# Optimization experiments

Measured on AMD Instinct MI355X. Metric: run time of the kernel, lower is better.

## Reference

```python
import jax, jax.numpy as jnp
import numpy as np

N_NODES = 100000
N_EDGES = 640000
F = 128          # in_features
MID = 192        # (2*F + OUT)//2
OUT = 128


def setup_inputs() -> dict:
    key = jax.random.key(0)
    k_h, k_dr, k_s, k_d, k_w1, k_w2 = jax.random.split(key, 6)
    h = jax.random.normal(k_h, (N_NODES, F), dtype=jnp.float32)
    dR = jax.random.uniform(k_dr, (N_EDGES,), dtype=jnp.float32)
    src_idx = jax.random.randint(k_s, (N_EDGES,), 0, N_NODES)
    dst_idx = jax.random.randint(k_d, (N_EDGES,), 0, N_NODES)
    W1 = jax.random.normal(k_w1, (2 * F + 1, MID), dtype=jnp.float32) * (1.0 / np.sqrt(2 * F + 1))
    b1 = jnp.zeros((MID,), dtype=jnp.float32)
    W2 = jax.random.normal(k_w2, (MID, OUT), dtype=jnp.float32) * (1.0 / np.sqrt(MID))
    b2 = jnp.zeros((OUT,), dtype=jnp.float32)
    return {"h": h, "dR": dR, "src_idx": src_idx, "dst_idx": dst_idx,
            "W1": W1, "b1": b1, "W2": W2, "b2": b2}


def reference(h, dR, src_idx, dst_idx, W1, b1, W2, b2):
    # first=True branch: cat([dst_hidden, src_hidden, dR[:, None]]) -> [E, 2F+1]
    inp = jnp.concatenate([h[dst_idx], h[src_idx], dR[:, None]], axis=1)
    hid = jax.nn.relu(inp @ W1 + b1)          # [E, MID]
    out = jnp.tanh(hid @ W2 + b2)             # [E, OUT]
    return out
```

## Files before the change

### kernel.cpp

```cpp
#include <hip/hip_runtime.h>


#define F_IN   128
#define MID    192
#define OUT_N  128
#define K1     256
#define M_TILE 64
#define H_STRIDE 200

typedef __attribute__((ext_vector_type(8))) short bf16x8;
typedef __attribute__((ext_vector_type(8))) unsigned short u16x8;
typedef __attribute__((ext_vector_type(4))) float f32x4;

__device__ __forceinline__ unsigned short f2bf(float f) {
    unsigned u = __builtin_bit_cast(unsigned, f);
    u = (u + 0x7FFFu + ((u >> 16) & 1u)) >> 16;
    return (unsigned short)u;
}

__global__ void pack_weights(const float* __restrict__ W1,
                             const float* __restrict__ W2,
                             unsigned short* __restrict__ p1,
                             unsigned short* __restrict__ p2,
                             float* __restrict__ wdr) {
    int i = blockIdx.x * 256 + threadIdx.x;
    if (i < K1 * MID) {
        int kin = i & 31;
        int rest = i >> 5;
        int n = rest % MID;
        int kt = rest / MID;
        p1[i] = f2bf(W1[(kt * 32 + kin) * MID + n]);
    }
    int j = i - K1 * MID;
    if (j >= 0 && j < MID * OUT_N) {
        int kin = j & 31;
        int rest = j >> 5;
        int n = rest & 127;
        int kt = rest >> 7;
        p2[j] = f2bf(W2[(kt * 32 + kin) * OUT_N + n]);
    }
    if (i < MID) wdr[i] = W1[256 * MID + i];
}

__global__ void hconv(const float* __restrict__ h,
                      unsigned short* __restrict__ hb, int n8) {
    int i = blockIdx.x * 256 + threadIdx.x;
    if (i >= n8) return;
    const float4* hp = (const float4*)h;
    float4 v0 = hp[2 * i];
    float4 v1 = hp[2 * i + 1];
    u16x8 o;
    o[0] = f2bf(v0.x); o[1] = f2bf(v0.y); o[2] = f2bf(v0.z); o[3] = f2bf(v0.w);
    o[4] = f2bf(v1.x); o[5] = f2bf(v1.y); o[6] = f2bf(v1.z); o[7] = f2bf(v1.w);
    *((u16x8*)hb + i) = o;
}

__global__ __launch_bounds__(256, 5)
void edge_mlp_kernel(const unsigned short* __restrict__ hb,
                     const float* __restrict__ dR,
                     const int*   __restrict__ src_idx,
                     const int*   __restrict__ dst_idx,
                     const float* __restrict__ b1,
                     const float* __restrict__ b2,
                     const unsigned short* __restrict__ p1,
                     const unsigned short* __restrict__ p2,
                     const float* __restrict__ wdr,
                     float* __restrict__ out) {
    __shared__ __align__(16) unsigned short sA[M_TILE * 256];

    const int tid  = threadIdx.x;
    const int lane = tid & 63;
    const int w    = tid >> 6;
    const int e0   = blockIdx.x * M_TILE;

    const float dr_own = dR[e0 + lane];

    {
        const int g = lane >> 4;
        const int c = lane & 15;
        const int part = g & 1;
        const int* __restrict__ ip = part ? src_idx : dst_idx;
        const int eb = w * 16 + (g >> 1);
        int rows[8];
#pragma unroll
        for (int i = 0; i < 8; ++i) rows[i] = ip[e0 + eb + 2 * i];
#pragma unroll
        for (int i = 0; i < 8; ++i) {
            const int el = eb + 2 * i;
            const unsigned short* gp =
                hb + ((size_t)rows[i] << 7) + ((c ^ (el & 7)) << 3);
            unsigned short* lp = &sA[(w * 16 + 2 * i) * 256];
            __builtin_amdgcn_global_load_lds(
                (const __attribute__((address_space(1))) void*)gp,
                (__attribute__((address_space(3))) void*)lp,
                16, 0, 0);
        }
    }
    __syncthreads();

    const int l15 = lane & 15;
    const int q   = lane >> 4;

    f32x4 acc1[4][3] = {};
    for (int kt = 0; kt < 8; ++kt) {
        bf16x8 a[4];
#pragma unroll
        for (int m = 0; m < 4; ++m) {
            const int r = m * 16 + l15;
            a[m] = *(const bf16x8*)(&sA[r * 256 + (((kt * 4 + q) ^ (r & 7)) << 3)]);
        }
#pragma unroll
        for (int ni = 0; ni < 3; ++ni) {
            const int nb = (w + ni * 4) * 16 + l15;
            bf16x8 bf = *(const bf16x8*)(&p1[((kt * MID + nb) << 5) + (q << 3)]);
#pragma unroll
            for (int m = 0; m < 4; ++m)
                acc1[m][ni] = __builtin_amdgcn_mfma_f32_16x16x32_bf16(a[m], bf, acc1[m][ni], 0, 0, 0);
        }
    }
    __syncthreads();

    float drv[16];
#pragma unroll
    for (int m = 0; m < 4; ++m)
#pragma unroll
        for (int r = 0; r < 4; ++r)
            drv[m * 4 + r] = __shfl(dr_own, m * 16 + q * 4 + r);

    unsigned short* sH = sA;
#pragma unroll
    for (int ni = 0; ni < 3; ++ni) {
        const int n = (w + ni * 4) * 16 + l15;
        const float bb = b1[n];
        const float wd = wdr[n];
#pragma unroll
        for (int m = 0; m < 4; ++m) {
#pragma unroll
            for (int r = 0; r < 4; ++r) {
                const int e = m * 16 + q * 4 + r;
                float v = acc1[m][ni][r] + bb + drv[m * 4 + r] * wd;
                v = fmaxf(v, 0.0f);
                sH[e * H_STRIDE + n] = f2bf(v);
            }
        }
    }
    __syncthreads();

    f32x4 acc2[4][2] = {};
    for (int kt = 0; kt < 6; ++kt) {
        bf16x8 a[4];
#pragma unroll
        for (int m = 0; m < 4; ++m)
            a[m] = *(const bf16x8*)(&sH[(m * 16 + l15) * H_STRIDE + kt * 32 + q * 8]);
#pragma unroll
        for (int ni = 0; ni < 2; ++ni) {
            const int nb = (w + ni * 4) * 16 + l15;
            bf16x8 bf = *(const bf16x8*)(&p2[((kt * OUT_N + nb) << 5) + (q << 3)]);
#pragma unroll
            for (int m = 0; m < 4; ++m)
                acc2[m][ni] = __builtin_amdgcn_mfma_f32_16x16x32_bf16(a[m], bf, acc2[m][ni], 0, 0, 0);
        }
    }

#pragma unroll
    for (int ni = 0; ni < 2; ++ni) {
        const int n = (w + ni * 4) * 16 + l15;
        const float bb = b2[n];
#pragma unroll
        for (int m = 0; m < 4; ++m) {
#pragma unroll
            for (int r = 0; r < 4; ++r) {
                const int e = e0 + m * 16 + q * 4 + r;
                float x = acc2[m][ni][r] + bb;
                x = fminf(fmaxf(x, -10.0f), 10.0f);
                float t = __expf(2.0f * x);
                float y = (t - 1.0f) * __builtin_amdgcn_rcpf(t + 1.0f);
                __builtin_nontemporal_store(y, &out[(size_t)e * OUT_N + n]);
            }
        }
    }
}

extern "C" void kernel_launch(void* const* d_in, const int* in_sizes, int n_in,
                              void* d_out, int out_size, void* d_ws, size_t ws_size,
                              hipStream_t stream) {
    const float* h   = (const float*)d_in[0];
    const float* dR  = (const float*)d_in[1];
    const int* src   = (const int*)d_in[2];
    const int* dst   = (const int*)d_in[3];
    const float* W1  = (const float*)d_in[4];
    const float* b1  = (const float*)d_in[5];
    const float* W2  = (const float*)d_in[6];
    const float* b2  = (const float*)d_in[7];
    float* out       = (float*)d_out;

    const int hn = in_sizes[0];
    const int E  = in_sizes[1];

    unsigned short* hbuf = (unsigned short*)d_ws;
    unsigned short* p1   = hbuf + hn;
    unsigned short* p2   = p1 + K1 * MID;
    float* wdr           = (float*)(p2 + MID * OUT_N);

    hconv<<<(hn / 8 + 255) / 256, 256, 0, stream>>>(h, hbuf, hn / 8);
    pack_weights<<<(K1 * MID + MID * OUT_N + 255) / 256, 256, 0, stream>>>(W1, W2, p1, p2, wdr);
    edge_mlp_kernel<<<E / M_TILE, 256, 0, stream>>>(hbuf, dR, src, dst, b1, b2, p1, p2, wdr, out);
}
```

Baseline: 503.9 us.

## Make edge MLP persistent with double-buffered gather and register-resident weights

Converts the edge MLP kernel into a persistent grid of 512 blocks that loop over tiles, prefetching the next tile's gathered node rows into a second LDS buffer while computing the current one. W1/W2 fragments and biases are loaded once into registers per block instead of per tile. This aims to hide gather latency and remove repeated weight loads, at the cost of high register pressure (occupancy lowered to 2 blocks per CU), doubled LDS, and dropping the nontemporal output stores.

```diff
diff --git a/kernel.cpp b/kernel.cpp
--- a/kernel.cpp
+++ b/kernel.cpp
@@ -7,6 +7,7 @@
 #define K1     256
 #define M_TILE 64
 #define H_STRIDE 200
+#define NBLK   512
 
 typedef __attribute__((ext_vector_type(8))) short bf16x8;
 typedef __attribute__((ext_vector_type(8))) unsigned short u16x8;
@@ -55,7 +56,11 @@
     *((u16x8*)hb + i) = o;
 }
 
-__global__ __launch_bounds__(256, 5)
+#define SBAR()  do { __builtin_amdgcn_sched_barrier(0); \
+                     __builtin_amdgcn_s_barrier();      \
+                     __builtin_amdgcn_sched_barrier(0); } while (0)
+
+__global__ __launch_bounds__(256, 2)
 void edge_mlp_kernel(const unsigned short* __restrict__ hb,
                      const float* __restrict__ dR,
                      const int*   __restrict__ src_idx,
@@ -65,118 +70,173 @@
                      const unsigned short* __restrict__ p1,
                      const unsigned short* __restrict__ p2,
                      const float* __restrict__ wdr,
-                     float* __restrict__ out) {
-    __shared__ __align__(16) unsigned short sA[M_TILE * 256];
+                     float* __restrict__ out,
+                     int NT) {
+    __shared__ __align__(16) unsigned short sA[2][M_TILE * 256];
 
     const int tid  = threadIdx.x;
     const int lane = tid & 63;
     const int w    = tid >> 6;
-    const int e0   = blockIdx.x * M_TILE;
-
-    const float dr_own = dR[e0 + lane];
-
+    const int l15  = lane & 15;
+    const int q    = lane >> 4;
+
+    const int g    = lane >> 4;
+    const int c    = lane & 15;
+    const int part = g & 1;
+    const int* __restrict__ ip = part ? src_idx : dst_idx;
+    const int eb   = w * 16 + (g >> 1);
+
+    bf16x8 w1f[8][3];
+#pragma unroll
+    for (int kt = 0; kt < 8; ++kt)
+#pragma unroll
+        for (int ni = 0; ni < 3; ++ni) {
+            const int nb = (w + ni * 4) * 16 + l15;
+            w1f[kt][ni] = *(const bf16x8*)(&p1[((kt * MID + nb) << 5) + (q << 3)]);
+        }
+    bf16x8 w2f[6][2];
+#pragma unroll
+    for (int kt = 0; kt < 6; ++kt)
+#pragma unroll
+        for (int ni = 0; ni < 2; ++ni) {
+            const int nb = (w + ni * 4) * 16 + l15;
+            w2f[kt][ni] = *(const bf16x8*)(&p2[((kt * OUT_N + nb) << 5) + (q << 3)]);
+        }
+    float bb1[3], wd1[3], bb2[2];
+#pragma unroll
+    for (int ni = 0; ni < 3; ++ni) {
+        const int n = (w + ni * 4) * 16 + l15;
+        bb1[ni] = b1[n]; wd1[ni] = wdr[n];
+    }
+#pragma unroll
+    for (int ni = 0; ni < 2; ++ni) bb2[ni] = b2[(w + ni * 4) * 16 + l15];
+
+    const int t0 = blockIdx.x;
+    if (t0 >= NT) return;
+
+    int idxc[8];
     {
-        const int g = lane >> 4;
-        const int c = lane & 15;
-        const int part = g & 1;
-        const int* __restrict__ ip = part ? src_idx : dst_idx;
-        const int eb = w * 16 + (g >> 1);
-        int rows[8];
-#pragma unroll
-        for (int i = 0; i < 8; ++i) rows[i] = ip[e0 + eb + 2 * i];
+        const int base = t0 * M_TILE + eb;
+#pragma unroll
+        for (int i = 0; i < 8; ++i) idxc[i] = ip[base + 2 * i];
 #pragma unroll
         for (int i = 0; i < 8; ++i) {
             const int el = eb + 2 * i;
             const unsigned short* gp =
-                hb + ((size_t)rows[i] << 7) + ((c ^ (el & 7)) << 3);
-            unsigned short* lp = &sA[(w * 16 + 2 * i) * 256];
+                hb + ((size_t)idxc[i] << 7) + ((c ^ (el & 7)) << 3);
+            unsigned short* lp = &sA[0][(w * 16 + 2 * i) * 256];
             __builtin_amdgcn_global_load_lds(
                 (const __attribute__((address_space(1))) void*)gp,
-                (__attribute__((address_space(3))) void*)lp,
-                16, 0, 0);
-        }
-    }
-    __syncthreads();
-
-    const int l15 = lane & 15;
-    const int q   = lane >> 4;
-
-    f32x4 acc1[4][3] = {};
-    for (int kt = 0; kt < 8; ++kt) {
-        bf16x8 a[4];
-#pragma unroll
-        for (int m = 0; m < 4; ++m) {
-            const int r = m * 16 + l15;
-            a[m] = *(const bf16x8*)(&sA[r * 256 + (((kt * 4 + q) ^ (r & 7)) << 3)]);
-        }
+                (__attribute__((address_space(3))) void*)lp, 16, 0, 0);
+        }
+    }
+    int t1 = t0 + NBLK; if (t1 > NT - 1) t1 = NT - 1;
+    {
+        const int base = t1 * M_TILE + eb;
+#pragma unroll
+        for (int i = 0; i < 8; ++i) idxc[i] = ip[base + 2 * i];
+    }
+    float dr_now = dR[t0 * M_TILE + lane];
+    float dr_nxt = dR[t1 * M_TILE + lane];
+
+    int cur = 0;
+    for (int t = t0; t < NT; t += NBLK, cur ^= 1) {
+#pragma unroll
+        for (int i = 0; i < 8; ++i) {
+            const int el = eb + 2 * i;
+            const unsigned short* gp =
+                hb + ((size_t)idxc[i] << 7) + ((c ^ (el & 7)) << 3);
+            unsigned short* lp = &sA[cur ^ 1][(w * 16 + 2 * i) * 256];
+            __builtin_amdgcn_global_load_lds(
+                (const __attribute__((address_space(1))) void*)gp,
+                (__attribute__((address_space(3))) void*)lp, 16, 0, 0);
+        }
+        {
+            int t2 = t + 2 * NBLK; if (t2 > NT - 1) t2 = NT - 1;
+            const int base = t2 * M_TILE + eb;
+#pragma unroll
+            for (int i = 0; i < 8; ++i) idxc[i] = ip[base + 2 * i];
+        }
+        SBAR();
+
+        const unsigned short* sAc = &sA[cur][0];
+        f32x4 acc1[4][3] = {};
+#pragma unroll
+        for (int kt = 0; kt < 8; ++kt) {
+            bf16x8 a[4];
+#pragma unroll
+            for (int m = 0; m < 4; ++m) {
+                const int r = m * 16 + l15;
+                a[m] = *(const bf16x8*)(&sAc[r * 256 + (((kt * 4 + q) ^ (r & 7)) << 3)]);
+            }
+#pragma unroll
+            for (int ni = 0; ni < 3; ++ni)
+#pragma unroll
+                for (int m = 0; m < 4; ++m)
+                    acc1[m][ni] = __builtin_amdgcn_mfma_f32_16x16x32_bf16(
+                        a[m], w1f[kt][ni], acc1[m][ni], 0, 0, 0);
+        }
+        SBAR();
+
+        float drv[16];
+#pragma unroll
+        for (int m = 0; m < 4; ++m)
+#pragma unroll
+            for (int r = 0; r < 4; ++r)
+                drv[m * 4 + r] = __shfl(dr_now, m * 16 + q * 4 + r);
+
+        unsigned short* sH = &sA[cur][0];
 #pragma unroll
         for (int ni = 0; ni < 3; ++ni) {
-            const int nb = (w + ni * 4) * 16 + l15;
-            bf16x8 bf = *(const bf16x8*)(&p1[((kt * MID + nb) << 5) + (q << 3)]);
+            const int n = (w + ni * 4) * 16 + l15;
 #pragma unroll
             for (int m = 0; m < 4; ++m)
-                acc1[m][ni] = __builtin_amdgcn_mfma_f32_16x16x32_bf16(a[m], bf, acc1[m][ni], 0, 0, 0);
-        }
-    }
-    __syncthreads();
-
-    float drv[16];
-#pragma unroll
-    for (int m = 0; m < 4; ++m)
-#pragma unroll
-        for (int r = 0; r < 4; ++r)
-            drv[m * 4 + r] = __shfl(dr_own, m * 16 + q * 4 + r);
-
-    unsigned short* sH = sA;
-#pragma unroll
-    for (int ni = 0; ni < 3; ++ni) {
-        const int n = (w + ni * 4) * 16 + l15;
-        const float bb = b1[n];
-        const float wd = wdr[n];
-#pragma unroll
-        for (int m = 0; m < 4; ++m) {
-#pragma unroll
-            for (int r = 0; r < 4; ++r) {
-                const int e = m * 16 + q * 4 + r;
-                float v = acc1[m][ni][r] + bb + drv[m * 4 + r] * wd;
-                v = fmaxf(v, 0.0f);
-                sH[e * H_STRIDE + n] = f2bf(v);
-            }
-        }
-    }
-    __syncthreads();
-
-    f32x4 acc2[4][2] = {};
-    for (int kt = 0; kt < 6; ++kt) {
-        bf16x8 a[4];
-#pragma unroll
-        for (int m = 0; m < 4; ++m)
-            a[m] = *(const bf16x8*)(&sH[(m * 16 + l15) * H_STRIDE + kt * 32 + q * 8]);
+#pragma unroll
+                for (int r = 0; r < 4; ++r) {
+                    const int e = m * 16 + q * 4 + r;
+                    float v = acc1[m][ni][r] + bb1[ni] + drv[m * 4 + r] * wd1[ni];
+                    v = fmaxf(v, 0.0f);
+                    sH[e * H_STRIDE + n] = f2bf(v);
+                }
+        }
+        asm volatile("s_waitcnt lgkmcnt(0)" ::: "memory");
+        SBAR();
+
+        f32x4 acc2[4][2] = {};
+#pragma unroll
+        for (int kt = 0; kt < 6; ++kt) {
+            bf16x8 a[4];
+#pragma unroll
+            for (int m = 0; m < 4; ++m)
+                a[m] = *(const bf16x8*)(&sH[(m * 16 + l15) * H_STRIDE + kt * 32 + q * 8]);
+#pragma unroll
+            for (int ni = 0; ni < 2; ++ni)
+#pragma unroll
+                for (int m = 0; m < 4; ++m)
+                    acc2[m][ni] = __builtin_amdgcn_mfma_f32_16x16x32_bf16(
+                        a[m], w2f[kt][ni], acc2[m][ni], 0, 0, 0);
+        }
+        SBAR();
+
 #pragma unroll
         for (int ni = 0; ni < 2; ++ni) {
-            const int nb = (w + ni * 4) * 16 + l15;
-            bf16x8 bf = *(const bf16x8*)(&p2[((kt * OUT_N + nb) << 5) + (q << 3)]);
+            const int n = (w + ni * 4) * 16 + l15;
 #pragma unroll
             for (int m = 0; m < 4; ++m)
-                acc2[m][ni] = __builtin_amdgcn_mfma_f32_16x16x32_bf16(a[m], bf, acc2[m][ni], 0, 0, 0);
-        }
-    }
-
-#pragma unroll
-    for (int ni = 0; ni < 2; ++ni) {
-        const int n = (w + ni * 4) * 16 + l15;
-        const float bb = b2[n];
-#pragma unroll
-        for (int m = 0; m < 4; ++m) {
-#pragma unroll
-            for (int r = 0; r < 4; ++r) {
-                const int e = e0 + m * 16 + q * 4 + r;
-                float x = acc2[m][ni][r] + bb;
-                x = fminf(fmaxf(x, -10.0f), 10.0f);
-                float t = __expf(2.0f * x);
-                float y = (t - 1.0f) * __builtin_amdgcn_rcpf(t + 1.0f);
-                __builtin_nontemporal_store(y, &out[(size_t)e * OUT_N + n]);
-            }
+#pragma unroll
+                for (int r = 0; r < 4; ++r) {
+                    const int e = t * M_TILE + m * 16 + q * 4 + r;
+                    float x = acc2[m][ni][r] + bb2[ni];
+                    x = fminf(fmaxf(x, -10.0f), 10.0f);
+                    float tt = __expf(2.0f * x);
+                    out[(size_t)e * OUT_N + n] = (tt - 1.0f) * __builtin_amdgcn_rcpf(tt + 1.0f);
+                }
+        }
+
+        dr_now = dr_nxt;
+        {
+            int t2 = t + 2 * NBLK; if (t2 > NT - 1) t2 = NT - 1;
+            dr_nxt = dR[t2 * M_TILE + lane];
         }
     }
 }
@@ -196,6 +256,7 @@
 
     const int hn = in_sizes[0];
     const int E  = in_sizes[1];
+    const int NT = E / M_TILE;
 
     unsigned short* hbuf = (unsigned short*)d_ws;
     unsigned short* p1   = hbuf + hn;
@@ -204,5 +265,7 @@
 
     hconv<<<(hn / 8 + 255) / 256, 256, 0, stream>>>(h, hbuf, hn / 8);
     pack_weights<<<(K1 * MID + MID * OUT_N + 255) / 256, 256, 0, stream>>>(W1, W2, p1, p2, wdr);
-    edge_mlp_kernel<<<E / M_TILE, 256, 0, stream>>>(hbuf, dR, src, dst, b1, b2, p1, p2, wdr, out);
-}
+
+    const int grid = NT < NBLK ? NT : NBLK;
+    edge_mlp_kernel<<<grid, 256, 0, stream>>>(hbuf, dR, src, dst, b1, b2, p1, p2, wdr, out, NT);
+}
```

Result: no change. 503.4 us (-0.1%).

## Swap MFMA operand roles so outputs are feature-contiguous for vector stores

Applied to the files above, without the earlier changes.

Both MFMA GEMMs now take the weight tile as the A operand and the edge features as the B operand, computing the transposed product. Each lane's four accumulator values then map to four consecutive output features of one edge. This lets the hidden layer be written to LDS as packed 8-byte stores and the final tanh output as 16-byte float4 global stores, instead of scattered scalar stores. Bias and dR-weight loads also become vector loads. The nontemporal store hint is dropped, and each wave now owns a contiguous range of output columns.

```diff
diff --git a/kernel.cpp b/kernel.cpp
--- a/kernel.cpp
+++ b/kernel.cpp
@@ -11,6 +11,7 @@
 typedef __attribute__((ext_vector_type(8))) short bf16x8;
 typedef __attribute__((ext_vector_type(8))) unsigned short u16x8;
 typedef __attribute__((ext_vector_type(4))) float f32x4;
+typedef __attribute__((ext_vector_type(2))) unsigned int u32x2;
 
 __device__ __forceinline__ unsigned short f2bf(float f) {
     unsigned u = __builtin_bit_cast(unsigned, f);
@@ -71,6 +72,8 @@
     const int tid  = threadIdx.x;
     const int lane = tid & 63;
     const int w    = tid >> 6;
+    const int l15  = lane & 15;
+    const int q    = lane >> 4;
     const int e0   = blockIdx.x * M_TILE;
 
     const float dr_own = dR[e0 + lane];
@@ -92,91 +95,95 @@
             unsigned short* lp = &sA[(w * 16 + 2 * i) * 256];
             __builtin_amdgcn_global_load_lds(
                 (const __attribute__((address_space(1))) void*)gp,
-                (__attribute__((address_space(3))) void*)lp,
-                16, 0, 0);
+                (__attribute__((address_space(3))) void*)lp, 16, 0, 0);
         }
     }
     __syncthreads();
 
-    const int l15 = lane & 15;
-    const int q   = lane >> 4;
-
-    f32x4 acc1[4][3] = {};
+    f32x4 acc1[3][4] = {};
     for (int kt = 0; kt < 8; ++kt) {
-        bf16x8 a[4];
-#pragma unroll
-        for (int m = 0; m < 4; ++m) {
-            const int r = m * 16 + l15;
-            a[m] = *(const bf16x8*)(&sA[r * 256 + (((kt * 4 + q) ^ (r & 7)) << 3)]);
-        }
-#pragma unroll
-        for (int ni = 0; ni < 3; ++ni) {
-            const int nb = (w + ni * 4) * 16 + l15;
-            bf16x8 bf = *(const bf16x8*)(&p1[((kt * MID + nb) << 5) + (q << 3)]);
-#pragma unroll
-            for (int m = 0; m < 4; ++m)
-                acc1[m][ni] = __builtin_amdgcn_mfma_f32_16x16x32_bf16(a[m], bf, acc1[m][ni], 0, 0, 0);
-        }
+        bf16x8 bfr[4];
+#pragma unroll
+        for (int et = 0; et < 4; ++et) {
+            const int r = et * 16 + l15;
+            bfr[et] = *(const bf16x8*)(&sA[r * 256 + (((kt * 4 + q) ^ (r & 7)) << 3)]);
+        }
+        bf16x8 w1a[3];
+#pragma unroll
+        for (int mi = 0; mi < 3; ++mi) {
+            const int nb = (3 * w + mi) * 16 + l15;
+            w1a[mi] = *(const bf16x8*)(&p1[((kt * MID + nb) << 5) + (q << 3)]);
+        }
+#pragma unroll
+        for (int mi = 0; mi < 3; ++mi)
+#pragma unroll
+            for (int et = 0; et < 4; ++et)
+                acc1[mi][et] = __builtin_amdgcn_mfma_f32_16x16x32_bf16(
+                    w1a[mi], bfr[et], acc1[mi][et], 0, 0, 0);
     }
     __syncthreads();
 
-    float drv[16];
-#pragma unroll
-    for (int m = 0; m < 4; ++m)
-#pragma unroll
-        for (int r = 0; r < 4; ++r)
-            drv[m * 4 + r] = __shfl(dr_own, m * 16 + q * 4 + r);
+    float drl[4];
+#pragma unroll
+    for (int et = 0; et < 4; ++et) drl[et] = __shfl(dr_own, et * 16 + l15);
 
     unsigned short* sH = sA;
 #pragma unroll
-    for (int ni = 0; ni < 3; ++ni) {
-        const int n = (w + ni * 4) * 16 + l15;
-        const float bb = b1[n];
-        const float wd = wdr[n];
-#pragma unroll
-        for (int m = 0; m < 4; ++m) {
+    for (int mi = 0; mi < 3; ++mi) {
+        const int n0 = (3 * w + mi) * 16 + q * 4;
+        const f32x4 bb = *(const f32x4*)(b1 + n0);
+        const f32x4 wd = *(const f32x4*)(wdr + n0);
+#pragma unroll
+        for (int et = 0; et < 4; ++et) {
+            const int e = et * 16 + l15;
+            float v0 = fmaxf(acc1[mi][et][0] + bb[0] + drl[et] * wd[0], 0.0f);
+            float v1 = fmaxf(acc1[mi][et][1] + bb[1] + drl[et] * wd[1], 0.0f);
+            float v2 = fmaxf(acc1[mi][et][2] + bb[2] + drl[et] * wd[2], 0.0f);
+            float v3 = fmaxf(acc1[mi][et][3] + bb[3] + drl[et] * wd[3], 0.0f);
+            u32x2 pk;
+            pk[0] = (unsigned)f2bf(v0) | ((unsigned)f2bf(v1) << 16);
+            pk[1] = (unsigned)f2bf(v2) | ((unsigned)f2bf(v3) << 16);
+            *(u32x2*)(&sH[e * H_STRIDE + n0]) = pk;
+        }
+    }
+    __syncthreads();
+
+    f32x4 acc2[2][4] = {};
+    for (int kt = 0; kt < 6; ++kt) {
+        bf16x8 hfr[4];
+#pragma unroll
+        for (int et = 0; et < 4; ++et)
+            hfr[et] = *(const bf16x8*)(&sH[(et * 16 + l15) * H_STRIDE + kt * 32 + q * 8]);
+        bf16x8 w2a[2];
+#pragma unroll
+        for (int mi = 0; mi < 2; ++mi) {
+            const int nb = (2 * w + mi) * 16 + l15;
+            w2a[mi] = *(const bf16x8*)(&p2[((kt * OUT_N + nb) << 5) + (q << 3)]);
+        }
+#pragma unroll
+        for (int mi = 0; mi < 2; ++mi)
+#pragma unroll
+            for (int et = 0; et < 4; ++et)
+                acc2[mi][et] = __builtin_amdgcn_mfma_f32_16x16x32_bf16(
+                    w2a[mi], hfr[et], acc2[mi][et], 0, 0, 0);
+    }
+
+#pragma unroll
+    for (int mi = 0; mi < 2; ++mi) {
+        const int n0 = (2 * w + mi) * 16 + q * 4;
+        const f32x4 bb2 = *(const f32x4*)(b2 + n0);
+#pragma unroll
+        for (int et = 0; et < 4; ++et) {
+            const size_t e = (size_t)(e0 + et * 16 + l15);
+            f32x4 y;
 #pragma unroll
             for (int r = 0; r < 4; ++r) {
-                const int e = m * 16 + q * 4 + r;
-                float v = acc1[m][ni][r] + bb + drv[m * 4 + r] * wd;
-                v = fmaxf(v, 0.0f);
-                sH[e * H_STRIDE + n] = f2bf(v);
+                float x = acc2[mi][et][r] + bb2[r];
+                x = fminf(fmaxf(x, -10.0f), 10.0f);
+                float tt = __expf(2.0f * x);
+                y[r] = (tt - 1.0f) * __builtin_amdgcn_rcpf(tt + 1.0f);
             }
-        }
-    }
-    __syncthreads();
-
-    f32x4 acc2[4][2] = {};
-    for (int kt = 0; kt < 6; ++kt) {
-        bf16x8 a[4];
-#pragma unroll
-        for (int m = 0; m < 4; ++m)
-            a[m] = *(const bf16x8*)(&sH[(m * 16 + l15) * H_STRIDE + kt * 32 + q * 8]);
-#pragma unroll
-        for (int ni = 0; ni < 2; ++ni) {
-            const int nb = (w + ni * 4) * 16 + l15;
-            bf16x8 bf = *(const bf16x8*)(&p2[((kt * OUT_N + nb) << 5) + (q << 3)]);
-#pragma unroll
-            for (int m = 0; m < 4; ++m)
-                acc2[m][ni] = __builtin_amdgcn_mfma_f32_16x16x32_bf16(a[m], bf, acc2[m][ni], 0, 0, 0);
-        }
-    }
-
-#pragma unroll
-    for (int ni = 0; ni < 2; ++ni) {
-        const int n = (w + ni * 4) * 16 + l15;
-        const float bb = b2[n];
-#pragma unroll
-        for (int m = 0; m < 4; ++m) {
-#pragma unroll
-            for (int r = 0; r < 4; ++r) {
-                const int e = e0 + m * 16 + q * 4 + r;
-                float x = acc2[m][ni][r] + bb;
-                x = fminf(fmaxf(x, -10.0f), 10.0f);
-                float t = __expf(2.0f * x);
-                float y = (t - 1.0f) * __builtin_amdgcn_rcpf(t + 1.0f);
-                __builtin_nontemporal_store(y, &out[(size_t)e * OUT_N + n]);
-            }
+            *(f32x4*)(out + e * OUT_N + n0) = y;
         }
     }
 }
```

Result: slower. 521.0 us (+3.4%).
